# Performance work log

Hardware: AMD Instinct MI355X
Metric: run time of the kernel (lower is better)

Reference implementation:

```python
import jax, jax.numpy as jnp
import numpy as np

B, S, SE, H, NH = 1, 2048, 2048, 1024, 16
HD = H // NH
INNER = 4 * H
EPS = 1e-5


def layer_norm(x, g, b):
    mu = jnp.mean(x, axis=-1, keepdims=True)
    var = jnp.mean(jnp.square(x - mu), axis=-1, keepdims=True)
    return (x - mu) * jax.lax.rsqrt(var + EPS) * g + b


def split_heads(x):  # [B,T,H] -> [B,NH,T,HD]
    b, t, _ = x.shape
    return x.reshape(b, t, NH, HD).transpose(0, 2, 1, 3)


def merge_heads(x):  # [B,NH,T,HD] -> [B,T,H]
    b, nh, t, hd = x.shape
    return x.transpose(0, 2, 1, 3).reshape(b, t, nh * hd)


def setup_inputs() -> dict:
    key = jax.random.key(0)
    ks = jax.random.split(key, 16)
    n = lambda k, shp: (jax.random.normal(k, shp, jnp.float32) * 0.02)
    return {
        "hidden_states": jax.random.normal(ks[0], (B, S, H), jnp.float32),
        "encoder_hidden_states": jax.random.normal(ks[1], (B, SE, H), jnp.float32),
        "scorer_logits": jax.random.normal(ks[2], (B, SE), jnp.float32),
        "ln1_g": jnp.ones((H,), jnp.float32), "ln1_b": jnp.zeros((H,), jnp.float32),
        "c_attn_w": n(ks[3], (H, 3 * H)), "c_attn_b": jnp.zeros((3 * H,), jnp.float32),
        "attn_proj_w": n(ks[4], (H, H)), "attn_proj_b": jnp.zeros((H,), jnp.float32),
        "lnx_g": jnp.ones((H,), jnp.float32), "lnx_b": jnp.zeros((H,), jnp.float32),
        "q_attn_w": n(ks[5], (H, H)), "q_attn_b": jnp.zeros((H,), jnp.float32),
        "x_kv_w": n(ks[6], (H, 2 * H)), "x_kv_b": jnp.zeros((2 * H,), jnp.float32),
        "x_proj_w": n(ks[7], (H, H)), "x_proj_b": jnp.zeros((H,), jnp.float32),
        "ln2_g": jnp.ones((H,), jnp.float32), "ln2_b": jnp.zeros((H,), jnp.float32),
        "fc_w": n(ks[8], (H, INNER)), "fc_b": jnp.zeros((INNER,), jnp.float32),
        "mlp_proj_w": n(ks[9], (INNER, H)), "mlp_proj_b": jnp.zeros((H,), jnp.float32),
    }


def _attn_core(q, k, v, extra_bias=None, causal_bool=False, tril_diag2_additive=False):
    # q,k,v: [B,NH,T,HD]; eager attention, materializes full score matrix (faithful to source)
    w = jnp.einsum("bhqd,bhkd->bhqk", q, k) / jnp.sqrt(jnp.asarray(HD, q.dtype))
    ql, kl = q.shape[-2], k.shape[-2]
    neg = jnp.finfo(w.dtype).min
    if causal_bool:
        mask = jnp.tril(jnp.ones((ql, kl), bool))  # self-attn boolean causal mask
        w = jnp.where(mask[None, None], w, neg)
    if tril_diag2_additive:
        cm = jnp.tril(jnp.ones((ql, kl), w.dtype), k=2)  # limit_cross_attn: tril diagonal=2
        w = w + jnp.where(cm == 0, neg, jnp.zeros((), w.dtype))[None, None]
    if extra_bias is not None:
        w = w + extra_bias[:, None, None, :]  # scorer_logits additive per-key bias
    w = jax.nn.softmax(w, axis=-1)
    return jnp.einsum("bhqk,bhkd->bhqd", w, v)


def reference(hidden_states, encoder_hidden_states, scorer_logits,
              ln1_g, ln1_b, c_attn_w, c_attn_b, attn_proj_w, attn_proj_b,
              lnx_g, lnx_b, q_attn_w, q_attn_b, x_kv_w, x_kv_b, x_proj_w, x_proj_b,
              ln2_g, ln2_b, fc_w, fc_b, mlp_proj_w, mlp_proj_b):
    # --- self attention ---
    residual = hidden_states
    x = layer_norm(hidden_states, ln1_g, ln1_b)
    qkv = x @ c_attn_w + c_attn_b
    q, k, v = jnp.split(qkv, 3, axis=-1)
    a = _attn_core(split_heads(q), split_heads(k), split_heads(v), causal_bool=True)
    a = merge_heads(a) @ attn_proj_w + attn_proj_b
    hidden_states = a + residual
    # --- cross attention (limit_cross_attn=True, scorer_logits bias) ---
    residual = hidden_states
    x = layer_norm(hidden_states, lnx_g, lnx_b)
    q = x @ q_attn_w + q_attn_b
    kv = encoder_hidden_states @ x_kv_w + x_kv_b
    k, v = jnp.split(kv, 2, axis=-1)
    a = _attn_core(split_heads(q), split_heads(k), split_heads(v),
                   extra_bias=scorer_logits, tril_diag2_additive=True)
    a = merge_heads(a) @ x_proj_w + x_proj_b
    hidden_states = residual + a
    # --- MLP (gelu_new = tanh approx) ---
    residual = hidden_states
    x = layer_norm(hidden_states, ln2_g, ln2_b)
    h = jax.nn.gelu(x @ fc_w + fc_b, approximate=True)
    hidden_states = residual + (h @ mlp_proj_w + mlp_proj_b)
    return hidden_states
```

## Files before the change

### kernel.cpp

```cpp
#include <hip/hip_runtime.h>
#include <stdint.h>

#define H     1024
#define S     2048
#define SEQE  2048
#define NHEAD 16
#define HD    64
#define INNER 4096
#define EPSLN 1e-5f
#define LOG2E 1.44269504089f
#define SCALE2 (0.125f * LOG2E)

typedef __attribute__((ext_vector_type(8))) short short8;
typedef __attribute__((ext_vector_type(4))) float floatx4;

__device__ __forceinline__ float b2f(unsigned short u){
  union { unsigned int i; float f; } v; v.i = ((unsigned int)u) << 16; return v.f;
}
__device__ __forceinline__ unsigned short f2b(float f){
  union { float f; unsigned int i; } v; v.f = f;
  unsigned int x = v.i;
  unsigned int r = (x + 0x7FFFu + ((x >> 16) & 1u)) >> 16;
  return (unsigned short)r;
}
__device__ __forceinline__ float gelu_tanh(float x){
  float x3 = x*x*x;
  float t = tanhf(0.7978845608028654f*(x + 0.044715f*x3));
  return 0.5f*x*(1.0f+t);
}

__device__ __forceinline__ void gld16(const unsigned short* g, unsigned short* l){
  __builtin_amdgcn_global_load_lds(
      (const __attribute__((address_space(1))) unsigned int*)g,
      (__attribute__((address_space(3))) unsigned int*)l,
      16, 0, 0);
}

__global__ __launch_bounds__(256) void k_sniff(
    const unsigned short* __restrict__ p, int* __restrict__ flag){
  __shared__ int any;
  if (threadIdx.x == 0) any = 0;
  __syncthreads();
  int bad = 0;
  for (int i = threadIdx.x; i < 8192; i += 256){
    float v = b2f(p[i]);
    if (!(fabsf(v) < 1e6f)) bad = 1;
  }
  if (bad) any = 1;
  __syncthreads();
  if (threadIdx.x == 0) flag[0] = any;
}

struct PrepT {
  const void* src[7];
  unsigned short* dst[7];
  int R[7], C[7];
  int pre[8];
};
__global__ __launch_bounds__(256) void k_prep_t(PrepT d, const int* __restrict__ flag){
  __shared__ unsigned short t[32][33];
  int b = blockIdx.x;
  int m = 0;
  while (b >= d.pre[m+1]) m++;
  int ti = b - d.pre[m];
  int R = d.R[m], C = d.C[m];
  int tx = threadIdx.x & 31, ty = threadIdx.x >> 5;
  int tilesx = C >> 5;
  int bc = (ti % tilesx) << 5, br = (ti / tilesx) << 5;
  const float* sf = (const float*)d.src[m];
  const unsigned short* sb = (const unsigned short*)d.src[m];
  unsigned short* dst = d.dst[m];
  int fl = flag[0];
  #pragma unroll
  for (int i = 0; i < 4; i++){
    size_t idx = (size_t)(br + ty + i*8) * C + bc + tx;
    t[ty + i*8][tx] = fl ? f2b(sf[idx]) : sb[idx];
  }
  __syncthreads();
  #pragma unroll
  for (int i = 0; i < 4; i++)
    dst[(size_t)(bc + ty + i*8) * R + br + tx] = t[tx][ty + i*8];
}

struct SmallCvt {
  const void* src[16];
  unsigned short* dst[16];
  int n[16];
};
__global__ __launch_bounds__(256) void k_prep_c(
    const void* __restrict__ enc, unsigned short* __restrict__ enc_c,
    const void* __restrict__ hsv, float* __restrict__ hidden,
    SmallCvt sc, const int* __restrict__ flag){
  int b = blockIdx.x, tid = threadIdx.x;
  int fl = flag[0];
  if (b < 8192){
    int i = b*256 + tid;
    enc_c[i] = fl ? f2b(((const float*)enc)[i]) : ((const unsigned short*)enc)[i];
  } else if (b < 16384){
    int i = (b - 8192)*256 + tid;
    hidden[i] = fl ? ((const float*)hsv)[i] : b2f(((const unsigned short*)hsv)[i]);
  } else {
    int t = b - 16384;
    const float* sf = (const float*)sc.src[t];
    const unsigned short* sb = (const unsigned short*)sc.src[t];
    unsigned short* d = sc.dst[t];
    for (int i = tid; i < sc.n[t]; i += 256)
      d[i] = fl ? f2b(sf[i]) : sb[i];
  }
}

__global__ __launch_bounds__(256) void k_layernorm(
    const float* __restrict__ x,
    const unsigned short* __restrict__ g, const unsigned short* __restrict__ bb,
    unsigned short* __restrict__ y){
  __shared__ float scratch[4];
  int row = blockIdx.x, tid = threadIdx.x;
  float v[4];
  #pragma unroll
  for (int i=0;i<4;i++) v[i] = x[(size_t)row*H + tid + i*256];
  float s = v[0]+v[1]+v[2]+v[3];
  for (int o=32;o;o>>=1) s += __shfl_xor(s,o,64);
  int wid = tid>>6, lane = tid&63;
  if (lane==0) scratch[wid]=s;
  __syncthreads();
  float mu = (scratch[0]+scratch[1]+scratch[2]+scratch[3]) * (1.0f/H);
  __syncthreads();
  float q = 0.f;
  #pragma unroll
  for (int i=0;i<4;i++){ float d=v[i]-mu; q += d*d; }
  for (int o=32;o;o>>=1) q += __shfl_xor(q,o,64);
  if (lane==0) scratch[wid]=q;
  __syncthreads();
  float var = (scratch[0]+scratch[1]+scratch[2]+scratch[3]) * (1.0f/H);
  float rstd = rsqrtf(var + EPSLN);
  #pragma unroll
  for (int i=0;i<4;i++){
    int idx = tid + i*256;
    float o = (v[i]-mu)*rstd*b2f(g[idx]) + b2f(bb[idx]);
    y[(size_t)row*H + idx] = f2b(o);
  }
}

__global__ __launch_bounds__(256) void k_gemm64(
    const unsigned short* __restrict__ A, const unsigned short* __restrict__ BT,
    const unsigned short* __restrict__ bias,
    unsigned short* __restrict__ outb, float* __restrict__ resid,
    int M, int N, int K, int mode, const int* __restrict__ flag,
    int vcol0, unsigned short* __restrict__ vtout)
{
  __shared__ __align__(16) unsigned short As[2][64*64];
  __shared__ __align__(16) unsigned short Bs[2][128*64];
  int tid = threadIdx.x;
  int bm0 = blockIdx.y * 64, bn0 = blockIdx.x * 128;
  int wid = tid >> 6, lane = tid & 63;
  int wm = (wid & 1) * 32, wn = (wid >> 1) * 64;
  int fl = (mode == 3) ? flag[0] : 0;
  floatx4 acc[2][4] = {};

  const unsigned short* gp[6];
  int lofs[6];
  int aseg[6];
  int lrow = lane >> 3, lchunk = (lane & 7) ^ lrow;
  #pragma unroll
  for (int t = 0; t < 6; t++){
    int seg = wid * 6 + t;
    if (seg < 8){
      gp[t] = A + (size_t)(bm0 + seg*8 + lrow) * K + lchunk*8;
      lofs[t] = seg * 512;
      aseg[t] = 1;
    } else {
      int s = seg - 8;
      gp[t] = BT + (size_t)(bn0 + s*8 + lrow) * K + lchunk*8;
      lofs[t] = s * 512;
      aseg[t] = 0;
    }
  }

  #pragma unroll
  for (int t = 0; t < 6; t++)
    gld16(gp[t], (aseg[t] ? As[0] : Bs[0]) + lofs[t]);

  int mrow = lane & 15, quad = lane >> 4;
  int ib = 0;
  for (int kt = 0; kt < K; kt += 64, ib ^= 1){
    __syncthreads();
    if (kt + 64 < K){
      #pragma unroll
      for (int t = 0; t < 6; t++)
        gld16(gp[t] + kt + 64, (aseg[t] ? As[ib^1] : Bs[ib^1]) + lofs[t]);
    }
    const unsigned short* Ac = As[ib];
    const unsigned short* Bc = Bs[ib];
    #pragma unroll
    for (int k2 = 0; k2 < 2; k2++){
      short8 af[2], bf[4];
      #pragma unroll
      for (int i = 0; i < 2; i++){
        int r = wm + i*16 + mrow;
        int slot = (k2*4 + quad) ^ (r & 7);
        af[i] = *(const short8*)&Ac[r*64 + slot*8];
      }
      #pragma unroll
      for (int j = 0; j < 4; j++){
        int r = wn + j*16 + mrow;
        int slot = (k2*4 + quad) ^ (r & 7);
        bf[j] = *(const short8*)&Bc[r*64 + slot*8];
      }
      #pragma unroll
      for (int i = 0; i < 2; i++){
        #pragma unroll
        for (int j = 0; j < 4; j++){
          acc[i][j] = __builtin_amdgcn_mfma_f32_16x16x32_bf16(af[i], bf[j], acc[i][j], 0,0,0);
        }
      }
    }
  }

  int colb = mrow, rowb = quad * 4;
  #pragma unroll
  for (int i=0;i<2;i++){
    #pragma unroll
    for (int j=0;j<4;j++){
      int col = bn0 + wn + j*16 + colb;
      float bv = b2f(bias[col]);
      int row0 = bm0 + wm + i*16 + rowb;
      if (mode == 4 && col >= vcol0){
        ushort4 uv;
        uv.x = f2b(acc[i][j][0] + bv);
        uv.y = f2b(acc[i][j][1] + bv);
        uv.z = f2b(acc[i][j][2] + bv);
        uv.w = f2b(acc[i][j][3] + bv);
        *(ushort4*)(vtout + (size_t)(col - vcol0)*M + row0) = uv;
      } else {
        #pragma unroll
        for (int rr=0;rr<4;rr++){
          int row = row0 + rr;
          float v = acc[i][j][rr] + bv;
          size_t off = (size_t)row*N + col;
          if      (mode == 0 || mode == 4){ outb[off] = f2b(v); }
          else if (mode == 1){ outb[off] = f2b(gelu_tanh(v)); }
          else if (mode == 2){ resid[off] += v; }
          else {
            float o = v + resid[off];
            if (fl) ((float*)outb)[off] = o;
            else    outb[off] = f2b(o);
          }
        }
      }
    }
  }
}

template<int CA, int SCOR>
__global__ __launch_bounds__(256) void k_flash2(
    const unsigned short* __restrict__ qb, int qstride,
    const unsigned short* __restrict__ kb, int kstride,
    const unsigned short* __restrict__ vt,
    const unsigned short* __restrict__ scorer,
    unsigned short* __restrict__ obuf, float* __restrict__ mlbuf, int TOTS)
{
  int t = blockIdx.x, h = blockIdx.y, sp = blockIdx.z;
  int klmax0 = 64*t + 64 + CA; if (klmax0 > S) klmax0 = S;
  int nch = (klmax0 + 63) >> 6;
  int nsp = (nch + 7) >> 3;
  if (sp >= nsp) return;
  int base = 0;
  for (int i = 0; i < t; i++){
    int km = 64*i + 64 + CA; if (km > S) km = S;
    base += (((km + 63) >> 6) + 7) >> 3;
  }
  int pidx = h*TOTS + base + sp;
  int c0 = sp*8, c1 = c0 + 8; if (c1 > nch) c1 = nch;

  __shared__ __align__(16) unsigned short Ks[2][64*64];
  __shared__ __align__(16) unsigned short VTs[2][64*64];
  __shared__ __align__(16) unsigned short Ps[4][16*72];
  __shared__ float scs[2][64];
  int tid = threadIdx.x;
  int q0 = t*64;
  int w = tid >> 6, lane = tid & 63;
  int cn = lane & 15, quad = lane >> 4, kq = quad * 8;
  unsigned short* Pw = Ps[w];
  int srow0 = w*16;
  int lr = lane >> 3;
  int lc = ((lane & 7) ^ lr) * 8;
  const unsigned short* kg0 = kb + (size_t)(srow0 + lr) * kstride + h*HD + lc;
  const unsigned short* kg1 = kb + (size_t)(srow0 + 8 + lr) * kstride + h*HD + lc;
  const unsigned short* vg0 = vt + (size_t)(h*HD + srow0 + lr) * S + lc;
  const unsigned short* vg1 = vt + (size_t)(h*HD + srow0 + 8 + lr) * S + lc;

  const unsigned short* qrow = qb + (size_t)(q0 + w*16 + cn) * qstride + h*HD;
  short8 qf0 = *(const short8*)(qrow + kq);
  short8 qf1 = *(const short8*)(qrow + kq + 32);
  floatx4 oacc[4] = {};
  float l_lane[4] = {0,0,0,0};
  float m_w = -1.0e38f;
  int qmr = q0 + w*16 + quad*4;

  {
    int kc = c0 * 64;
    gld16(kg0 + (size_t)kc * kstride, Ks[0] + srow0*64);
    gld16(kg1 + (size_t)kc * kstride, Ks[0] + (srow0 + 8)*64);
    gld16(vg0 + kc, VTs[0] + srow0*64);
    gld16(vg1 + kc, VTs[0] + (srow0 + 8)*64);
    if (SCOR && tid < 64) scs[0][tid] = b2f(scorer[kc + tid]) * LOG2E;
  }

  int ib = 0;
  for (int ci = c0; ci < c1; ci++, ib ^= 1){
    __syncthreads();
    if (ci + 1 < c1){
      int kn2 = (ci + 1) * 64;
      gld16(kg0 + (size_t)kn2 * kstride, Ks[ib^1] + srow0*64);
      gld16(kg1 + (size_t)kn2 * kstride, Ks[ib^1] + (srow0 + 8)*64);
      gld16(vg0 + kn2, VTs[ib^1] + srow0*64);
      gld16(vg1 + kn2, VTs[ib^1] + (srow0 + 8)*64);
      if (SCOR && tid < 64) scs[ib^1][tid] = b2f(scorer[kn2 + tid]) * LOG2E;
    }
    int kc = ci * 64;
    const unsigned short* Kc = Ks[ib];
    const unsigned short* Vc = VTs[ib];
    const float* scc = scs[ib];

    floatx4 sv[4] = {};
    #pragma unroll
    for (int t4=0;t4<4;t4++){
      int rr = t4*16 + cn;
      int s0 = ((quad    ) ^ (rr & 7)) * 8;
      int s1 = ((quad + 4) ^ (rr & 7)) * 8;
      short8 b0 = *(const short8*)&Kc[rr*64 + s0];
      short8 b1 = *(const short8*)&Kc[rr*64 + s1];
      sv[t4] = __builtin_amdgcn_mfma_f32_16x16x32_bf16(qf0, b0, sv[t4], 0,0,0);
      sv[t4] = __builtin_amdgcn_mfma_f32_16x16x32_bf16(qf1, b1, sv[t4], 0,0,0);
    }

    float vals[16];
    float lmax = -1.0e38f;
    if (kc + 63 > q0 + w*16 + CA){
      #pragma unroll
      for (int t4=0;t4<4;t4++){
        #pragma unroll
        for (int r=0;r<4;r++){
          float s = sv[t4][r] * SCALE2;
          if (SCOR) s += scc[t4*16 + cn];
          int kn = kc + t4*16 + cn;
          s = (kn <= qmr + r + CA) ? s : -1.0e38f;
          vals[t4*4+r] = s;
          lmax = fmaxf(lmax, s);
        }
      }
    } else {
      #pragma unroll
      for (int t4=0;t4<4;t4++){
        #pragma unroll
        for (int r=0;r<4;r++){
          float s = sv[t4][r] * SCALE2;
          if (SCOR) s += scc[t4*16 + cn];
          vals[t4*4+r] = s;
          lmax = fmaxf(lmax, s);
        }
      }
    }
    #pragma unroll
    for (int o=1;o<64;o<<=1) lmax = fmaxf(lmax, __shfl_xor(lmax, o, 64));
    if (lmax > m_w){
      float al = exp2f(m_w - lmax);
      m_w = lmax;
      #pragma unroll
      for (int r=0;r<4;r++) l_lane[r] *= al;
      #pragma unroll
      for (int t2=0;t2<4;t2++){
        #pragma unroll
        for (int r=0;r<4;r++) oacc[t2][r] *= al;
      }
    }
    #pragma unroll
    for (int t4=0;t4<4;t4++){
      #pragma unroll
      for (int r=0;r<4;r++){
        float e = exp2f(vals[t4*4+r] - m_w);
        l_lane[r] += e;
        Pw[(quad*4+r)*72 + t4*16 + cn] = f2b(e);
      }
    }
    short8 pf0 = *(const short8*)&Pw[cn*72 + kq];
    short8 pf1 = *(const short8*)&Pw[cn*72 + kq + 32];
    #pragma unroll
    for (int t2=0;t2<4;t2++){
      int rr = t2*16 + cn;
      int s0 = ((quad    ) ^ (rr & 7)) * 8;
      int s1 = ((quad + 4) ^ (rr & 7)) * 8;
      short8 v0 = *(const short8*)&Vc[rr*64 + s0];
      short8 v1 = *(const short8*)&Vc[rr*64 + s1];
      oacc[t2] = __builtin_amdgcn_mfma_f32_16x16x32_bf16(pf0, v0, oacc[t2], 0,0,0);
      oacc[t2] = __builtin_amdgcn_mfma_f32_16x16x32_bf16(pf1, v1, oacc[t2], 0,0,0);
    }
  }

  float lrow[4];
  #pragma unroll
  for (int r=0;r<4;r++){
    float l = l_lane[r];
    l += __shfl_xor(l,1,64); l += __shfl_xor(l,2,64);
    l += __shfl_xor(l,4,64); l += __shfl_xor(l,8,64);
    lrow[r] = l;
  }
  size_t ob = (size_t)pidx*4096 + (size_t)(w*16 + quad*4)*64;
  #pragma unroll
  for (int t2=0;t2<4;t2++){
    #pragma unroll
    for (int r=0;r<4;r++)
      obuf[ob + r*64 + t2*16 + cn] = f2b(oacc[t2][r]);
  }
  if (cn == 0){
    #pragma unroll
    for (int r=0;r<4;r++){
      int row64 = w*16 + quad*4 + r;
      mlbuf[((size_t)pidx*64 + row64)*2]   = m_w;
      mlbuf[((size_t)pidx*64 + row64)*2+1] = lrow[r];
    }
  }
}

template<int CA>
__global__ __launch_bounds__(256) void k_comb(
    const unsigned short* __restrict__ obuf, const float* __restrict__ mlbuf,
    unsigned short* __restrict__ out, int TOTS)
{
  int h = blockIdx.y;
  int row = blockIdx.x*16 + (threadIdx.x >> 4);
  int d0 = (threadIdx.x & 15) * 4;
  int t = row >> 6;
  int klmax0 = 64*t + 64 + CA; if (klmax0 > S) klmax0 = S;
  int nch = (klmax0 + 63) >> 6;
  int nsp = (nch + 7) >> 3;
  int base = 0;
  for (int i = 0; i < t; i++){
    int km = 64*i + 64 + CA; if (km > S) km = S;
    base += (((km + 63) >> 6) + 7) >> 3;
  }
  int row64 = row & 63;
  float mp[4], lp[4];
  float M = -1.0e38f;
  for (int p = 0; p < nsp; p++){
    int pi = h*TOTS + base + p;
    mp[p] = mlbuf[((size_t)pi*64 + row64)*2];
    lp[p] = mlbuf[((size_t)pi*64 + row64)*2+1];
    M = fmaxf(M, mp[p]);
  }
  float L = 0.f;
  float o0=0.f,o1=0.f,o2=0.f,o3=0.f;
  for (int p = 0; p < nsp; p++){
    int pi = h*TOTS + base + p;
    float wgt = exp2f(mp[p] - M);
    L += lp[p]*wgt;
    const unsigned short* op = obuf + (size_t)pi*4096 + row64*64 + d0;
    o0 += b2f(op[0])*wgt; o1 += b2f(op[1])*wgt;
    o2 += b2f(op[2])*wgt; o3 += b2f(op[3])*wgt;
  }
  float inv = 1.0f / L;
  size_t oo = (size_t)row*H + h*HD + d0;
  out[oo]   = f2b(o0*inv); out[oo+1] = f2b(o1*inv);
  out[oo+2] = f2b(o2*inv); out[oo+3] = f2b(o3*inv);
}

extern "C" void kernel_launch(void* const* d_in, const int* in_sizes, int n_in,
                              void* d_out, int out_size, void* d_ws, size_t ws_size,
                              hipStream_t stream)
{
  const void* hs          = d_in[0];
  const void* enc         = d_in[1];
  const void* scorer      = d_in[2];
  const void* ln1_g       = d_in[3];
  const void* ln1_b       = d_in[4];
  const void* c_attn_w    = d_in[5];
  const void* c_attn_b    = d_in[6];
  const void* attn_proj_w = d_in[7];
  const void* attn_proj_b = d_in[8];
  const void* lnx_g       = d_in[9];
  const void* lnx_b       = d_in[10];
  const void* q_attn_w    = d_in[11];
  const void* q_attn_b    = d_in[12];
  const void* x_kv_w      = d_in[13];
  const void* x_kv_b      = d_in[14];
  const void* x_proj_w    = d_in[15];
  const void* x_proj_b    = d_in[16];
  const void* ln2_g       = d_in[17];
  const void* ln2_b       = d_in[18];
  const void* fc_w        = d_in[19];
  const void* fc_b        = d_in[20];
  const void* mlp_proj_w  = d_in[21];
  const void* mlp_proj_b  = d_in[22];
  unsigned short* out = (unsigned short*)d_out;

  char* ws = (char*)d_ws; size_t off = 0;
  auto alloc = [&](size_t bytes)->void*{
    void* p = ws + off; off += (bytes + 255) & ~(size_t)255; return p;
  };
  unsigned short* wT_cattn = (unsigned short*)alloc((size_t)3072*1024*2);
  unsigned short* wT_aproj = (unsigned short*)alloc((size_t)1024*1024*2);
  unsigned short* wT_qattn = (unsigned short*)alloc((size_t)1024*1024*2);
  unsigned short* wT_xkv   = (unsigned short*)alloc((size_t)2048*1024*2);
  unsigned short* wT_xproj = (unsigned short*)alloc((size_t)1024*1024*2);
  unsigned short* wT_fc    = (unsigned short*)alloc((size_t)4096*1024*2);
  unsigned short* wT_mlp   = (unsigned short*)alloc((size_t)1024*4096*2);
  unsigned short* enc_c    = (unsigned short*)alloc((size_t)SEQE*H*2);
  unsigned short* canon    = (unsigned short*)alloc((size_t)32768*2);
  unsigned short* xln      = (unsigned short*)alloc((size_t)S*H*2);
  unsigned short* qkv      = (unsigned short*)alloc((size_t)S*3*H*2);
  unsigned short* attnout  = (unsigned short*)alloc((size_t)S*H*2);
  unsigned short* q2       = (unsigned short*)alloc((size_t)S*H*2);
  unsigned short* kvbuf    = (unsigned short*)alloc((size_t)SEQE*2*H*2);
  unsigned short* vt_self  = (unsigned short*)alloc((size_t)H*S*2);
  unsigned short* vt_cross = (unsigned short*)alloc((size_t)H*SEQE*2);
  unsigned short* fcbuf    = (unsigned short*)alloc((size_t)S*INNER*2);
  float*          hidden   = (float*)alloc((size_t)S*H*4);
  int*            flag     = (int*)alloc(256);

  unsigned short* obuf  = fcbuf;
  float*          mlbuf = (float*)(fcbuf + (size_t)16*83*4096);

  unsigned short* p = canon;
  auto carve = [&](int n)->unsigned short*{ unsigned short* q = p; p += n; return q; };
  unsigned short* c_ln1g = carve(1024); unsigned short* c_ln1b = carve(1024);
  unsigned short* c_catb = carve(3072); unsigned short* c_aprb = carve(1024);
  unsigned short* c_lnxg = carve(1024); unsigned short* c_lnxb = carve(1024);
  unsigned short* c_qatb = carve(1024); unsigned short* c_xkvb = carve(2048);
  unsigned short* c_xprb = carve(1024); unsigned short* c_ln2g = carve(1024);
  unsigned short* c_ln2b = carve(1024); unsigned short* c_fcb  = carve(4096);
  unsigned short* c_mlpb = carve(1024); unsigned short* c_scor = carve(2048);

  k_sniff<<<1, 256, 0, stream>>>((const unsigned short*)hs, flag);

  PrepT pt{};
  const void* tsrc[7] = {c_attn_w, attn_proj_w, q_attn_w, x_kv_w, x_proj_w, fc_w, mlp_proj_w};
  unsigned short* tdst[7] = {wT_cattn, wT_aproj, wT_qattn, wT_xkv, wT_xproj, wT_fc, wT_mlp};
  int tR[7] = {1024,1024,1024,1024,1024,1024,4096};
  int tC[7] = {3072,1024,1024,2048,1024,4096,1024};
  int acc_t = 0;
  for (int i=0;i<7;i++){
    pt.src[i]=tsrc[i]; pt.dst[i]=tdst[i]; pt.R[i]=tR[i]; pt.C[i]=tC[i];
    pt.pre[i]=acc_t; acc_t += (tC[i]>>5)*(tR[i]>>5);
  }
  pt.pre[7]=acc_t;
  k_prep_t<<<acc_t, 256, 0, stream>>>(pt, flag);

  SmallCvt sc{};
  const void* ssrc[14] = {ln1_g, ln1_b, c_attn_b, attn_proj_b, lnx_g, lnx_b,
                          q_attn_b, x_kv_b, x_proj_b, ln2_g, ln2_b, fc_b,
                          mlp_proj_b, scorer};
  unsigned short* sdst[14] = {c_ln1g, c_ln1b, c_catb, c_aprb, c_lnxg, c_lnxb,
                              c_qatb, c_xkvb, c_xprb, c_ln2g, c_ln2b, c_fcb,
                              c_mlpb, c_scor};
  int sn[14] = {1024,1024,3072,1024,1024,1024,1024,2048,1024,1024,1024,4096,1024,2048};
  for (int i=0;i<14;i++){ sc.src[i]=ssrc[i]; sc.dst[i]=sdst[i]; sc.n[i]=sn[i]; }
  k_prep_c<<<16384 + 14, 256, 0, stream>>>(enc, enc_c, hs, hidden, sc, flag);

  k_layernorm<<<S, 256, 0, stream>>>(hidden, c_ln1g, c_ln1b, xln);
  k_gemm64<<<dim3(3072/128, S/64), 256, 0, stream>>>(xln, wT_cattn, c_catb,
      qkv, nullptr, S, 3072, 1024, 4, flag, 2048, vt_self);
  k_flash2<0,0><<<dim3(32, NHEAD, 4), 256, 0, stream>>>(
      qkv, 3*H, qkv + 1024, 3*H, vt_self, nullptr, obuf, mlbuf, 80);
  k_comb<0><<<dim3(S/16, NHEAD), 256, 0, stream>>>(obuf, mlbuf, attnout, 80);
  k_gemm64<<<dim3(1024/128, S/64), 256, 0, stream>>>(attnout, wT_aproj, c_aprb,
      nullptr, hidden, S, 1024, 1024, 2, flag, 0, nullptr);

  k_layernorm<<<S, 256, 0, stream>>>(hidden, c_lnxg, c_lnxb, xln);
  k_gemm64<<<dim3(1024/128, S/64), 256, 0, stream>>>(xln, wT_qattn, c_qatb,
      q2, nullptr, S, 1024, 1024, 0, flag, 0, nullptr);
  k_gemm64<<<dim3(2048/128, SEQE/64), 256, 0, stream>>>(enc_c, wT_xkv, c_xkvb,
      kvbuf, nullptr, SEQE, 2048, 1024, 4, flag, 1024, vt_cross);
  k_flash2<2,1><<<dim3(32, NHEAD, 4), 256, 0, stream>>>(
      q2, H, kvbuf, 2*H, vt_cross, c_scor, obuf, mlbuf, 83);
  k_comb<2><<<dim3(S/16, NHEAD), 256, 0, stream>>>(obuf, mlbuf, attnout, 83);
  k_gemm64<<<dim3(1024/128, S/64), 256, 0, stream>>>(attnout, wT_xproj, c_xprb,
      nullptr, hidden, S, 1024, 1024, 2, flag, 0, nullptr);

  k_layernorm<<<S, 256, 0, stream>>>(hidden, c_ln2g, c_ln2b, xln);
  k_gemm64<<<dim3(INNER/128, S/64), 256, 0, stream>>>(xln, wT_fc, c_fcb,
      fcbuf, nullptr, S, INNER, 1024, 1, flag, 0, nullptr);
  k_gemm64<<<dim3(1024/128, S/64), 256, 0, stream>>>(fcbuf, wT_mlp, c_mlpb,
      out, hidden, S, 1024, INNER, 3, flag, 0, nullptr);
}
```

Before: 511.0 us.

## Add 64x64-tile GEMM for N=1024 projections and use native exp2 in attention

Adds a k_gemm64s kernel with 64x64 output tiles, double-buffered LDS loads and XOR-swizzled layout. It is used for the four N=1024 GEMMs (attention projections, q projection, MLP down projection) so the grid has twice as many blocks and fills more CUs on a 2048x1024 output. The flash-attention softmax now uses the hardware exp2 builtin instead of exp2f, and the row-max shuffle reduction drops the xor-16 and xor-32 steps. This assumes the max only needs reducing across 16 lanes, which changes semantics if other lanes held distinct rows' data. Smaller tiles give less data reuse per block.

```diff
diff --git a/kernel.cpp b/kernel.cpp
--- a/kernel.cpp
+++ b/kernel.cpp
@@ -23,6 +23,7 @@
   unsigned int r = (x + 0x7FFFu + ((x >> 16) & 1u)) >> 16;
   return (unsigned short)r;
 }
+__device__ __forceinline__ float fexp2(float x){ return __builtin_amdgcn_exp2f(x); }
 __device__ __forceinline__ float gelu_tanh(float x){
   float x3 = x*x*x;
   float t = tanhf(0.7978845608028654f*(x + 0.044715f*x3));
@@ -251,6 +252,97 @@
   }
 }
 
+__global__ __launch_bounds__(256) void k_gemm64s(
+    const unsigned short* __restrict__ A, const unsigned short* __restrict__ BT,
+    const unsigned short* __restrict__ bias,
+    unsigned short* __restrict__ outb, float* __restrict__ resid,
+    int M, int N, int K, int mode, const int* __restrict__ flag)
+{
+  __shared__ __align__(16) unsigned short As[2][64*64];
+  __shared__ __align__(16) unsigned short Bs[2][64*64];
+  int tid = threadIdx.x;
+  int bm0 = blockIdx.y * 64, bn0 = blockIdx.x * 64;
+  int wid = tid >> 6, lane = tid & 63;
+  int wm = wid * 16;
+  int fl = (mode == 3) ? flag[0] : 0;
+  floatx4 acc[4] = {};
+
+  const unsigned short* gp[4];
+  int lofs[4];
+  int aseg[4];
+  int lrow = lane >> 3, lchunk = (lane & 7) ^ lrow;
+  #pragma unroll
+  for (int t = 0; t < 4; t++){
+    int seg = wid * 4 + t;
+    if (seg < 8){
+      gp[t] = A + (size_t)(bm0 + seg*8 + lrow) * K + lchunk*8;
+      lofs[t] = seg * 512;
+      aseg[t] = 1;
+    } else {
+      int s = seg - 8;
+      gp[t] = BT + (size_t)(bn0 + s*8 + lrow) * K + lchunk*8;
+      lofs[t] = s * 512;
+      aseg[t] = 0;
+    }
+  }
+
+  #pragma unroll
+  for (int t = 0; t < 4; t++)
+    gld16(gp[t], (aseg[t] ? As[0] : Bs[0]) + lofs[t]);
+
+  int mrow = lane & 15, quad = lane >> 4;
+  int ib = 0;
+  for (int kt = 0; kt < K; kt += 64, ib ^= 1){
+    __syncthreads();
+    if (kt + 64 < K){
+      #pragma unroll
+      for (int t = 0; t < 4; t++)
+        gld16(gp[t] + kt + 64, (aseg[t] ? As[ib^1] : Bs[ib^1]) + lofs[t]);
+    }
+    const unsigned short* Ac = As[ib];
+    const unsigned short* Bc = Bs[ib];
+    #pragma unroll
+    for (int k2 = 0; k2 < 2; k2++){
+      short8 af, bf[4];
+      {
+        int r = wm + mrow;
+        int slot = (k2*4 + quad) ^ (r & 7);
+        af = *(const short8*)&Ac[r*64 + slot*8];
+      }
+      #pragma unroll
+      for (int j = 0; j < 4; j++){
+        int r = j*16 + mrow;
+        int slot = (k2*4 + quad) ^ (r & 7);
+        bf[j] = *(const short8*)&Bc[r*64 + slot*8];
+      }
+      #pragma unroll
+      for (int j = 0; j < 4; j++)
+        acc[j] = __builtin_amdgcn_mfma_f32_16x16x32_bf16(af, bf[j], acc[j], 0,0,0);
+    }
+  }
+
+  int colb = mrow, rowb = quad * 4;
+  #pragma unroll
+  for (int j=0;j<4;j++){
+    int col = bn0 + j*16 + colb;
+    float bv = b2f(bias[col]);
+    int row0 = bm0 + wm + rowb;
+    #pragma unroll
+    for (int rr=0;rr<4;rr++){
+      int row = row0 + rr;
+      float v = acc[j][rr] + bv;
+      size_t off = (size_t)row*N + col;
+      if      (mode == 0){ outb[off] = f2b(v); }
+      else if (mode == 2){ resid[off] += v; }
+      else {
+        float o = v + resid[off];
+        if (fl) ((float*)outb)[off] = o;
+        else    outb[off] = f2b(o);
+      }
+    }
+  }
+}
+
 template<int CA, int SCOR>
 __global__ __launch_bounds__(256) void k_flash2(
     const unsigned short* __restrict__ qb, int qstride,
@@ -361,10 +453,12 @@
         }
       }
     }
-    #pragma unroll
-    for (int o=1;o<64;o<<=1) lmax = fmaxf(lmax, __shfl_xor(lmax, o, 64));
+    lmax = fmaxf(lmax, __shfl_xor(lmax,1,64));
+    lmax = fmaxf(lmax, __shfl_xor(lmax,2,64));
+    lmax = fmaxf(lmax, __shfl_xor(lmax,4,64));
+    lmax = fmaxf(lmax, __shfl_xor(lmax,8,64));
     if (lmax > m_w){
-      float al = exp2f(m_w - lmax);
+      float al = fexp2(m_w - lmax);
       m_w = lmax;
       #pragma unroll
       for (int r=0;r<4;r++) l_lane[r] *= al;
@@ -378,7 +472,7 @@
     for (int t4=0;t4<4;t4++){
       #pragma unroll
       for (int r=0;r<4;r++){
-        float e = exp2f(vals[t4*4+r] - m_w);
+        float e = fexp2(vals[t4*4+r] - m_w);
         l_lane[r] += e;
         Pw[(quad*4+r)*72 + t4*16 + cn] = f2b(e);
       }
@@ -452,7 +546,7 @@
   float o0=0.f,o1=0.f,o2=0.f,o3=0.f;
   for (int p = 0; p < nsp; p++){
     int pi = h*TOTS + base + p;
-    float wgt = exp2f(mp[p] - M);
+    float wgt = fexp2(mp[p] - M);
     L += lp[p]*wgt;
     const unsigned short* op = obuf + (size_t)pi*4096 + row64*64 + d0;
     o0 += b2f(op[0])*wgt; o1 += b2f(op[1])*wgt;
@@ -562,23 +656,23 @@
   k_flash2<0,0><<<dim3(32, NHEAD, 4), 256, 0, stream>>>(
       qkv, 3*H, qkv + 1024, 3*H, vt_self, nullptr, obuf, mlbuf, 80);
   k_comb<0><<<dim3(S/16, NHEAD), 256, 0, stream>>>(obuf, mlbuf, attnout, 80);
-  k_gemm64<<<dim3(1024/128, S/64), 256, 0, stream>>>(attnout, wT_aproj, c_aprb,
-      nullptr, hidden, S, 1024, 1024, 2, flag, 0, nullptr);
+  k_gemm64s<<<dim3(1024/64, S/64), 256, 0, stream>>>(attnout, wT_aproj, c_aprb,
+      nullptr, hidden, S, 1024, 1024, 2, flag);
 
   k_layernorm<<<S, 256, 0, stream>>>(hidden, c_lnxg, c_lnxb, xln);
-  k_gemm64<<<dim3(1024/128, S/64), 256, 0, stream>>>(xln, wT_qattn, c_qatb,
-      q2, nullptr, S, 1024, 1024, 0, flag, 0, nullptr);
+  k_gemm64s<<<dim3(1024/64, S/64), 256, 0, stream>>>(xln, wT_qattn, c_qatb,
+      q2, nullptr, S, 1024, 1024, 0, flag);
   k_gemm64<<<dim3(2048/128, SEQE/64), 256, 0, stream>>>(enc_c, wT_xkv, c_xkvb,
       kvbuf, nullptr, SEQE, 2048, 1024, 4, flag, 1024, vt_cross);
   k_flash2<2,1><<<dim3(32, NHEAD, 4), 256, 0, stream>>>(
       q2, H, kvbuf, 2*H, vt_cross, c_scor, obuf, mlbuf, 83);
   k_comb<2><<<dim3(S/16, NHEAD), 256, 0, stream>>>(obuf, mlbuf, attnout, 83);
-  k_gemm64<<<dim3(1024/128, S/64), 256, 0, stream>>>(attnout, wT_xproj, c_xprb,
-      nullptr, hidden, S, 1024, 1024, 2, flag, 0, nullptr);
+  k_gemm64s<<<dim3(1024/64, S/64), 256, 0, stream>>>(attnout, wT_xproj, c_xprb,
+      nullptr, hidden, S, 1024, 1024, 2, flag);
 
   k_layernorm<<<S, 256, 0, stream>>>(hidden, c_ln2g, c_ln2b, xln);
   k_gemm64<<<dim3(INNER/128, S/64), 256, 0, stream>>>(xln, wT_fc, c_fcb,
       fcbuf, nullptr, S, INNER, 1024, 1, flag, 0, nullptr);
-  k_gemm64<<<dim3(1024/128, S/64), 256, 0, stream>>>(fcbuf, wT_mlp, c_mlpb,
-      out, hidden, S, 1024, INNER, 3, flag, 0, nullptr);
-}
+  k_gemm64s<<<dim3(1024/64, S/64), 256, 0, stream>>>(fcbuf, wT_mlp, c_mlpb,
+      out, hidden, S, 1024, INNER, 3, flag);
+}
```

New measurement: 467.1 us. -8.6%, faster.
